# Performance work log

Measured on AMD Instinct MI355X. Metric: run time of the kernel, lower is better.

## Reference

```python
import jax, jax.numpy as jnp
import numpy as np

B, E, DM = 2, 1024, 512          # batch, n_edges, d_model
H, DK, DV = 8, 64, 64            # heads, d_k, d_v
MAX_NEIGHBOR = 5                 # == attn_max_dist
LN_EPS = 1e-6
NEG = -1e9


def setup_inputs() -> dict:
    key = jax.random.key(0)
    ks = jax.random.split(key, 9)
    s = 0.02
    return {
        "x": jax.random.normal(ks[0], (B, DM, E, 1), jnp.float32),
        "dist": jax.random.randint(ks[1], (B, E, E), 0, 12, jnp.int32),
        "base_rpr": jax.random.normal(ks[2], (MAX_NEIGHBOR + 1, DK), jnp.float32) * s,
        "w_q": jax.random.normal(ks[3], (DM, H * DK), jnp.float32) * s,
        "w_k": jax.random.normal(ks[4], (DM, H * DK), jnp.float32) * s,
        "w_v": jax.random.normal(ks[5], (DM, H * DV), jnp.float32) * s,
        "w_fc": jax.random.normal(ks[6], (H * DV, DM), jnp.float32) * s,
        "ln_g": jnp.ones((DM,), jnp.float32),
        "ln_b": jnp.zeros((DM,), jnp.float32),
    }


def reference(x, dist, base_rpr, w_q, w_k, w_v, w_fc, ln_g, ln_b):
    temp = jnp.asarray(DK, x.dtype) ** 0.5
    # local-attention mask (dist <= attn_max_dist); all edges valid (same-size meshes)
    mask = dist <= MAX_NEIGHBOR                      # [B,E,E] bool

    s = jnp.transpose(x[..., 0], (0, 2, 1))          # [B,E,DM]
    residual = s

    # LayerNorm applied to q only (as in the torch module)
    mu = s.mean(-1, keepdims=True)
    var = ((s - mu) ** 2).mean(-1, keepdims=True)
    qn = (s - mu) / jnp.sqrt(var + LN_EPS) * ln_g + ln_b

    q = (qn @ w_q).reshape(B, E, H, DK).transpose(0, 2, 1, 3)   # [B,H,E,DK]
    k = (s @ w_k).reshape(B, E, H, DK).transpose(0, 2, 1, 3)
    v = (s @ w_v).reshape(B, E, H, DV).transpose(0, 2, 1, 3)

    # relative-position representations gathered by (clipped) distance
    rpr = base_rpr[jnp.minimum(dist, MAX_NEIGHBOR)]  # [B,E,E,DK]

    qs = q / temp
    attn1 = jnp.einsum("bhid,bhjd->bhij", qs, k)
    attn2 = jnp.einsum("bhid,bijd->bhij", qs, rpr)
    logits = jnp.where(mask[:, None], attn1 + attn2, NEG)
    attn = jax.nn.softmax(logits, axis=-1)           # [B,H,E,E]

    out = jnp.einsum("bhij,bhjd->bhid", attn, v)     # [B,H,E,DV]
    out = out.transpose(0, 2, 1, 3).reshape(B, E, H * DV) @ w_fc + residual
    x_out = out.transpose(0, 2, 1)[..., None]        # [B,DM,E,1]

    mf = mask[:, None].astype(attn.dtype)            # [B,1,E,E]
    attn_per_edge = (attn * mf).sum((1, 2)) / mf.sum((1, 2))  # [B,E]
    return x_out, attn, attn_per_edge
```

## Files before the change

### kernel.cpp

```cpp
#include <hip/hip_runtime.h>

#define NB_B 2
#define NB_E 1024
#define NB_DM 512
#define NB_H 8
#define NEGV -1e9f

typedef __attribute__((ext_vector_type(8))) __bf16 bf16x8;
typedef __attribute__((ext_vector_type(8))) unsigned short u16x8;
typedef __attribute__((ext_vector_type(4))) float f32x4;

static __device__ __forceinline__ float bf2f(unsigned short u){
  union { unsigned int i; float f; } v; v.i = ((unsigned int)u) << 16; return v.f;
}
static __device__ __forceinline__ unsigned short f2bf(float f){
  union { float f; unsigned int i; } v; v.f = f;
  unsigned int r = v.i + 0x7FFFu + ((v.i >> 16) & 1u);
  return (unsigned short)(r >> 16);
}
static __device__ __forceinline__ f32x4 mfma16(bf16x8 a, bf16x8 b, f32x4 c){
  return __builtin_amdgcn_mfma_f32_16x16x32_bf16(a, b, c, 0, 0, 0);
}
static __device__ __forceinline__ float fast_exp2(float x){
#if __has_builtin(__builtin_amdgcn_exp2f)
  return __builtin_amdgcn_exp2f(x);
#else
  return exp2f(x);
#endif
}

__global__ void k_transpose_x(const float* __restrict__ x, unsigned short* __restrict__ s_bf){
  __shared__ float tile[32][33];
  const int b = blockIdx.z;
  const int d0 = blockIdx.y * 32;
  const int e0 = blockIdx.x * 32;
  const int tx = threadIdx.x, ty = threadIdx.y;
  #pragma unroll
  for (int r = 0; r < 4; ++r){
    const int d = d0 + ty + r*8;
    tile[ty + r*8][tx] = x[((size_t)b*NB_DM + d)*NB_E + e0 + tx];
  }
  __syncthreads();
  #pragma unroll
  for (int r = 0; r < 4; ++r){
    const int e = e0 + ty + r*8;
    s_bf[((size_t)b*NB_E + e)*NB_DM + d0 + tx] = f2bf(tile[tx][ty + r*8]);
  }
}

__global__ void k_transpose_w(const float* __restrict__ w0, const float* __restrict__ w1,
                              const float* __restrict__ w2, const float* __restrict__ w3,
                              unsigned short* __restrict__ wT){
  __shared__ float tile[32][33];
  const int which = blockIdx.z;
  const float* w = which==0 ? w0 : which==1 ? w1 : which==2 ? w2 : w3;
  unsigned short* dst = wT + (size_t)which*512*512;
  const int k0 = blockIdx.y*32, n0 = blockIdx.x*32;
  const int tx = threadIdx.x, ty = threadIdx.y;
  #pragma unroll
  for (int r = 0; r < 4; ++r)
    tile[ty + r*8][tx] = w[(size_t)(k0 + ty + r*8)*512 + n0 + tx];
  __syncthreads();
  #pragma unroll
  for (int r = 0; r < 4; ++r)
    dst[(size_t)(n0 + ty + r*8)*512 + k0 + tx] = f2bf(tile[tx][ty + r*8]);
}

__global__ __launch_bounds__(256) void k_ln(const unsigned short* __restrict__ s_bf,
    unsigned short* __restrict__ qn_bf, const float* __restrict__ gg, const float* __restrict__ bb){
  const int row = blockIdx.x*4 + (threadIdx.x >> 6);
  const int l = threadIdx.x & 63;
  const unsigned short* sp = s_bf + (size_t)row*512 + l*8;
  u16x8 v = *(const u16x8*)sp;
  float f[8]; float sum = 0.f, sq = 0.f;
  #pragma unroll
  for (int i = 0; i < 8; ++i){ f[i] = bf2f(v[i]); sum += f[i]; sq += f[i]*f[i]; }
  #pragma unroll
  for (int off = 32; off >= 1; off >>= 1){
    sum += __shfl_xor(sum, off);
    sq  += __shfl_xor(sq, off);
  }
  const float mu  = sum * (1.f/512.f);
  const float var = sq * (1.f/512.f) - mu*mu;
  const float rstd = rsqrtf(var + 1e-6f);
  const float4 g0 = *(const float4*)(gg + l*8);
  const float4 g1 = *(const float4*)(gg + l*8 + 4);
  const float4 b0 = *(const float4*)(bb + l*8);
  const float4 b1 = *(const float4*)(bb + l*8 + 4);
  const float gv[8] = {g0.x,g0.y,g0.z,g0.w,g1.x,g1.y,g1.z,g1.w};
  const float bv[8] = {b0.x,b0.y,b0.z,b0.w,b1.x,b1.y,b1.z,b1.w};
  u16x8 o;
  #pragma unroll
  for (int i = 0; i < 8; ++i) o[i] = f2bf((f[i]-mu)*rstd*gv[i] + bv[i]);
  *(u16x8*)(qn_bf + (size_t)row*512 + l*8) = o;
}

__global__ __launch_bounds__(256) void k_dist(const int* __restrict__ dist,
    unsigned char* __restrict__ d8, int* __restrict__ cnt){
  const int b = blockIdx.y;
  const int i0 = blockIdx.x * 16;
  const int t = threadIdx.x;
  int c0 = 0, c1 = 0, c2 = 0, c3 = 0;
  #pragma unroll 4
  for (int r = 0; r < 16; ++r){
    const int row = i0 + r;
    const int4 d = ((const int4*)(dist + ((size_t)b*NB_E + row)*NB_E))[t];
    uchar4 o;
    o.x = (unsigned char)(d.x <= 5 ? d.x : 6);
    o.y = (unsigned char)(d.y <= 5 ? d.y : 6);
    o.z = (unsigned char)(d.z <= 5 ? d.z : 6);
    o.w = (unsigned char)(d.w <= 5 ? d.w : 6);
    ((uchar4*)(d8 + ((size_t)b*NB_E + row)*NB_E))[t] = o;
    c0 += (d.x <= 5); c1 += (d.y <= 5); c2 += (d.z <= 5); c3 += (d.w <= 5);
  }
  int* cb = cnt + b*NB_E + t*4;
  atomicAdd(cb + 0, c0);
  atomicAdd(cb + 1, c1);
  atomicAdd(cb + 2, c2);
  atomicAdd(cb + 3, c3);
}

__global__ __launch_bounds__(256, 4) void k_gemm_qkv(
    const unsigned short* __restrict__ qn, const unsigned short* __restrict__ s,
    const unsigned short* __restrict__ wT, const float* __restrict__ base_rpr,
    unsigned short* __restrict__ Qb, unsigned short* __restrict__ Kb,
    unsigned short* __restrict__ VTb, float* __restrict__ qr)
{
  const int z = blockIdx.z;
  const unsigned short* A  = (z == 0) ? qn : s;
  const unsigned short* BT = wT + (size_t)z*262144;
  const int tid = threadIdx.x;
  const int l = tid & 63, wv = tid >> 6;
  const int ll = l & 15, lg = l >> 4;
  const int m0 = blockIdx.x*64 + wv*16;
  const int n0 = blockIdx.y*64;
  const unsigned short* arow = A + (size_t)(m0 + ll)*512 + lg*8;
  const unsigned short* brow = BT + (size_t)(n0 + ll)*512 + lg*8;
  f32x4 acc[4];
  #pragma unroll
  for (int nt = 0; nt < 4; ++nt) acc[nt] = (f32x4){0.f,0.f,0.f,0.f};
  bf16x8 a_c = *(const bf16x8*)(arow);
  bf16x8 b_c[4];
  #pragma unroll
  for (int nt = 0; nt < 4; ++nt) b_c[nt] = *(const bf16x8*)(brow + (size_t)nt*8192);
  #pragma unroll
  for (int ks = 0; ks < 16; ++ks){
    const int kn = (ks + 1) & 15;
    bf16x8 a_n = *(const bf16x8*)(arow + kn*32);
    bf16x8 b_n[4];
    #pragma unroll
    for (int nt = 0; nt < 4; ++nt) b_n[nt] = *(const bf16x8*)(brow + (size_t)nt*8192 + kn*32);
    #pragma unroll
    for (int nt = 0; nt < 4; ++nt) acc[nt] = mfma16(a_c, b_c[nt], acc[nt]);
    a_c = a_n;
    #pragma unroll
    for (int nt = 0; nt < 4; ++nt) b_c[nt] = b_n[nt];
  }
  const int rbase = m0 + lg*4;
  const int bidx = rbase >> 10;
  const int e = rbase & 1023;
  const int h = n0 >> 6;
  if (z == 0){
    float rprv[6][4];
    #pragma unroll
    for (int c = 0; c < 6; ++c)
      #pragma unroll
      for (int nt = 0; nt < 4; ++nt)
        rprv[c][nt] = base_rpr[c*64 + nt*16 + ll];
    #pragma unroll
    for (int nt = 0; nt < 4; ++nt){
      const int dk = nt*16 + ll;
      unsigned short* dp = Qb + (((size_t)bidx*NB_H + h)*NB_E + e)*64 + dk;
      #pragma unroll
      for (int r = 0; r < 4; ++r)
        dp[(size_t)r*64] = f2bf(acc[nt][r]*0.125f);
    }
    #pragma unroll
    for (int r = 0; r < 4; ++r){
      #pragma unroll
      for (int c = 0; c < 6; ++c){
        float tv = 0.f;
        #pragma unroll
        for (int nt = 0; nt < 4; ++nt) tv += acc[nt][r]*0.125f*rprv[c][nt];
        tv += __shfl_xor(tv, 1);
        tv += __shfl_xor(tv, 2);
        tv += __shfl_xor(tv, 4);
        tv += __shfl_xor(tv, 8);
        if (ll == 0)
          qr[(((size_t)(bidx*NB_H + h)*NB_E) + e + r)*8 + c] = tv;
      }
    }
  } else if (z == 1){
    #pragma unroll
    for (int nt = 0; nt < 4; ++nt){
      const int dk = nt*16 + ll;
      unsigned short* dp = Kb + (((size_t)bidx*NB_H + h)*NB_E + e)*64 + dk;
      #pragma unroll
      for (int r = 0; r < 4; ++r)
        dp[(size_t)r*64] = f2bf(acc[nt][r]);
    }
  } else {
    #pragma unroll
    for (int nt = 0; nt < 4; ++nt){
      const int dv = nt*16 + ll;
      ushort4 ov;
      ov.x = f2bf(acc[nt][0]); ov.y = f2bf(acc[nt][1]);
      ov.z = f2bf(acc[nt][2]); ov.w = f2bf(acc[nt][3]);
      *(ushort4*)(VTb + (((size_t)bidx*NB_H + h)*64 + dv)*NB_E + e) = ov;
    }
  }
}

__global__ __launch_bounds__(256, 4) void k_fc(
    const unsigned short* __restrict__ A, const unsigned short* __restrict__ BT,
    float* __restrict__ dst_f, const float* __restrict__ resid)
{
  const int tid = threadIdx.x;
  const int l = tid & 63, wv = tid >> 6;
  const int ll = l & 15, lg = l >> 4;
  const int m0 = blockIdx.x*64 + wv*16;
  const int n0 = blockIdx.y*32;
  const unsigned short* arow = A + (size_t)(m0 + ll)*512 + lg*8;
  const unsigned short* brow = BT + (size_t)(n0 + ll)*512 + lg*8;
  f32x4 acc[2];
  acc[0] = (f32x4){0.f,0.f,0.f,0.f};
  acc[1] = (f32x4){0.f,0.f,0.f,0.f};
  bf16x8 a_c = *(const bf16x8*)(arow);
  bf16x8 b_c0 = *(const bf16x8*)(brow);
  bf16x8 b_c1 = *(const bf16x8*)(brow + 8192);
  #pragma unroll
  for (int ks = 0; ks < 16; ++ks){
    const int kn = (ks + 1) & 15;
    bf16x8 a_n  = *(const bf16x8*)(arow + kn*32);
    bf16x8 b_n0 = *(const bf16x8*)(brow + kn*32);
    bf16x8 b_n1 = *(const bf16x8*)(brow + 8192 + kn*32);
    acc[0] = mfma16(a_c, b_c0, acc[0]);
    acc[1] = mfma16(a_c, b_c1, acc[1]);
    a_c = a_n; b_c0 = b_n0; b_c1 = b_n1;
  }
  const int rbase = m0 + lg*4;
  const int bidx = rbase >> 10;
  const int e = rbase & 1023;
  #pragma unroll
  for (int nt = 0; nt < 2; ++nt){
    const int n = n0 + nt*16 + ll;
    const float* xr = resid + ((size_t)bidx*NB_DM + n)*NB_E + e;
    const float4 rv = *(const float4*)xr;
    const float4 ov = make_float4(acc[nt][0]+rv.x, acc[nt][1]+rv.y,
                                  acc[nt][2]+rv.z, acc[nt][3]+rv.w);
    *(float4*)(dst_f + ((size_t)bidx*NB_DM + n)*NB_E + e) = ov;
  }
}

#define D_OFF 2048
#define P_OFF 18432
__global__ __launch_bounds__(256, 3) void k_attn(
    const unsigned short* __restrict__ Q, const unsigned short* __restrict__ K,
    const unsigned short* __restrict__ VT, const float* __restrict__ qr,
    const unsigned char* __restrict__ d8, float* __restrict__ attn_out,
    unsigned short* __restrict__ outb, float* __restrict__ ape_acc)
{
  __shared__ __align__(16) unsigned char smem[51200];
  unsigned short* plds = (unsigned short*)(smem + P_OFF);
  float* qr_l = (float*)smem;
  float* redm = (float*)(smem + 512);
  float* reds = (float*)(smem + 1024);

  const int tid = threadIdx.x;
  const int l = tid & 63, w = tid >> 6;
  const int lg = l >> 4, ll = l & 15;
  const int n = blockIdx.x;
  const int m = n >> 3;
  const int bh = (n & 7)*2 + (m >> 6);
  const int b = bh >> 3;
  const int ib = (m & 63) << 4;

  const unsigned char* d8g = d8 + ((size_t)b*NB_E + ib)*NB_E;
  int4 dreg[4];
  #pragma unroll
  for (int ch = 0; ch < 4; ++ch)
    dreg[ch] = ((const int4*)(d8g + (size_t)ch*4096))[tid];

  for (int t = tid; t < 16*6; t += 256)
    qr_l[t] = qr[((size_t)bh*NB_E + ib + (t/6))*8 + (t % 6)];

  const unsigned short* Qb = Q + ((size_t)bh*NB_E + ib)*64;
  bf16x8 qf[2];
  #pragma unroll
  for (int hf = 0; hf < 2; ++hf)
    qf[hf] = *(const bf16x8*)(Qb + (size_t)ll*64 + hf*32 + lg*8);

  f32x4 s[16];
  const unsigned short* Kb = K + (size_t)bh*NB_E*64;
  bf16x8 k0 = *(const bf16x8*)(Kb + (size_t)((w*16)*16 + ll)*64 + lg*8);
  bf16x8 k1 = *(const bf16x8*)(Kb + (size_t)((w*16)*16 + ll)*64 + 32 + lg*8);
  #pragma unroll
  for (int jt = 0; jt < 16; ++jt){
    const int jn = (jt + 1) & 15;
    const size_t nrow = (size_t)((w*16 + jn)*16 + ll)*64;
    bf16x8 kn0 = *(const bf16x8*)(Kb + nrow + lg*8);
    bf16x8 kn1 = *(const bf16x8*)(Kb + nrow + 32 + lg*8);
    f32x4 acc = {0.f,0.f,0.f,0.f};
    acc = mfma16(qf[0], k0, acc);
    acc = mfma16(qf[1], k1, acc);
    s[jt] = acc;
    k0 = kn0; k1 = kn1;
  }

  #pragma unroll
  for (int ch = 0; ch < 4; ++ch)
    ((int4*)(smem + D_OFF + ch*4096))[tid] = dreg[ch];
  __syncthreads();

  #pragma unroll
  for (int jt = 0; jt < 16; ++jt){
    const int j = (w*16 + jt)*16 + ll;
    #pragma unroll
    for (int r = 0; r < 4; ++r){
      const int il = lg*4 + r;
      const unsigned char c = smem[D_OFF + il*1024 + j];
      s[jt][r] = (c < 6) ? (s[jt][r] + qr_l[il*6 + c]) : NEGV;
    }
  }

  #pragma unroll
  for (int r = 0; r < 4; ++r){
    float mm = -3.0e38f;
    #pragma unroll
    for (int jt = 0; jt < 16; ++jt) mm = fmaxf(mm, s[jt][r]);
    mm = fmaxf(mm, __shfl_xor(mm, 1));
    mm = fmaxf(mm, __shfl_xor(mm, 2));
    mm = fmaxf(mm, __shfl_xor(mm, 4));
    mm = fmaxf(mm, __shfl_xor(mm, 8));
    if (ll == 0) redm[w*16 + lg*4 + r] = mm;
  }
  __syncthreads();
  float mx[4];
  #pragma unroll
  for (int r = 0; r < 4; ++r){
    const int il = lg*4 + r;
    mx[r] = fmaxf(fmaxf(redm[il], redm[16+il]), fmaxf(redm[32+il], redm[48+il]));
  }

  #pragma unroll
  for (int r = 0; r < 4; ++r){
    float sum = 0.f;
    #pragma unroll
    for (int jt = 0; jt < 16; ++jt){
      const float p = fast_exp2((s[jt][r] - mx[r]) * 1.4426950408889634f);
      s[jt][r] = p;
      sum += p;
    }
    sum += __shfl_xor(sum, 1);
    sum += __shfl_xor(sum, 2);
    sum += __shfl_xor(sum, 4);
    sum += __shfl_xor(sum, 8);
    if (ll == 0) reds[w*16 + lg*4 + r] = sum;
  }
  __syncthreads();
  float rinv[4];
  #pragma unroll
  for (int r = 0; r < 4; ++r){
    const int il = lg*4 + r;
    rinv[r] = 1.0f / (reds[il] + reds[16+il] + reds[32+il] + reds[48+il]);
  }

  #pragma unroll
  for (int jt = 0; jt < 16; ++jt){
    const int j = (w*16 + jt)*16 + ll;
    float csum = 0.f;
    #pragma unroll
    for (int r = 0; r < 4; ++r){
      const int il = lg*4 + r;
      const float pn = s[jt][r] * rinv[r];
      const int byo = ((il*1024 + j)*2) ^ ((il & 7) << 4);
      plds[byo >> 1] = f2bf(pn);
      csum += pn;
    }
    csum += __shfl_xor(csum, 16);
    csum += __shfl_xor(csum, 32);
    if (l < 16) atomicAdd(&ape_acc[(bh << 10) + j], csum);
  }
  __syncthreads();

  {
    const int il = w*4 + lg;
    float* arow = attn_out + ((size_t)bh*NB_E + ib + il)*NB_E;
    const int rowb = il*2048;
    #pragma unroll
    for (int c2 = 0; c2 < 16; ++c2){
      const int byo = (rowb + c2*128 + ll*8) ^ ((il & 7) << 4);
      const ushort4 pv = *(const ushort4*)(smem + P_OFF + byo);
      f32x4 ov;
      ov[0] = bf2f(pv.x); ov[1] = bf2f(pv.y); ov[2] = bf2f(pv.z); ov[3] = bf2f(pv.w);
      __builtin_nontemporal_store(ov, (f32x4*)(arow + c2*64 + ll*4));
    }
  }

  const unsigned short* Vb = VT + ((size_t)bh*64 + w*16 + ll)*NB_E;
  f32x4 o = {0.f,0.f,0.f,0.f};
  bf16x8 vf = *(const bf16x8*)(Vb + lg*8);
  #pragma unroll
  for (int kk = 0; kk < 32; ++kk){
    const int kn = (kk + 1) & 31;
    bf16x8 vn = *(const bf16x8*)(Vb + kn*32 + lg*8);
    const int byo = ((ll*2048 + (kk*32 + lg*8)*2)) ^ ((ll & 7) << 4);
    bf16x8 p = *(const bf16x8*)(smem + P_OFF + byo);
    o = mfma16(p, vf, o);
    vf = vn;
  }
  const int coln = (bh & 7)*64 + w*16 + ll;
  #pragma unroll
  for (int r = 0; r < 4; ++r){
    const int e0 = ib + lg*4 + r;
    outb[((size_t)b*NB_E + e0)*512 + coln] = f2bf(o[r]);
  }
}

__global__ void k_ape(const float* __restrict__ acc, const int* __restrict__ cnt,
                      float* __restrict__ out){
  const int t = blockIdx.x*256 + threadIdx.x;
  if (t < NB_B*NB_E){
    const int b = t >> 10, j = t & 1023;
    float ssum = 0.f;
    #pragma unroll
    for (int h = 0; h < 8; ++h) ssum += acc[(((b<<3) + h) << 10) + j];
    const int c = cnt[t];
    out[t] = c > 0 ? ssum / (float)c : 0.f;
  }
}

extern "C" void kernel_launch(void* const* d_in, const int* in_sizes, int n_in,
                              void* d_out, int out_size, void* d_ws, size_t ws_size,
                              hipStream_t stream)
{
  const float* x        = (const float*)d_in[0];
  const int*   dist     = (const int*)d_in[1];
  const float* base_rpr = (const float*)d_in[2];
  const float* w_q      = (const float*)d_in[3];
  const float* w_k      = (const float*)d_in[4];
  const float* w_v      = (const float*)d_in[5];
  const float* w_fc     = (const float*)d_in[6];
  const float* ln_g     = (const float*)d_in[7];
  const float* ln_b     = (const float*)d_in[8];

  float* x_out    = (float*)d_out;
  float* attn_out = x_out + (size_t)NB_B*NB_DM*NB_E;
  float* ape_out  = attn_out + (size_t)NB_B*NB_H*NB_E*NB_E;

  unsigned char* ws = (unsigned char*)d_ws;
  unsigned short* s_bf   = (unsigned short*)(ws);
  unsigned short* qn_bf  = (unsigned short*)(ws + 2097152);
  unsigned short* wT     = (unsigned short*)(ws + 4194304);
  unsigned short* Qb     = (unsigned short*)(ws + 6291456);
  unsigned short* Kb     = (unsigned short*)(ws + 8388608);
  unsigned short* VTb    = (unsigned short*)(ws + 10485760);
  unsigned short* outb   = (unsigned short*)(ws + 12582912);
  float*          qr     = (float*)(ws + 14680064);
  unsigned char*  d8     = ws + 15204352;
  int*            cnt    = (int*)(ws + 17301504);
  float*          apeacc = (float*)(ws + 17309696);

  hipMemsetAsync(cnt, 0, 8192 + 65536, stream);

  k_transpose_w<<<dim3(16,16,4), dim3(32,8), 0, stream>>>(w_q, w_k, w_v, w_fc, wT);
  k_transpose_x<<<dim3(32,16,2), dim3(32,8), 0, stream>>>(x, s_bf);
  k_ln<<<dim3(512), dim3(256), 0, stream>>>(s_bf, qn_bf, ln_g, ln_b);
  k_dist<<<dim3(64,2), dim3(256), 0, stream>>>(dist, d8, cnt);

  k_gemm_qkv<<<dim3(32,8,3), dim3(256), 0, stream>>>(qn_bf, s_bf, wT, base_rpr,
                                                     Qb, Kb, VTb, qr);

  k_attn<<<dim3(1024), dim3(256), 0, stream>>>(Qb, Kb, VTb, qr, d8, attn_out, outb, apeacc);

  k_fc<<<dim3(32,16), dim3(256), 0, stream>>>(outb, wT + 786432, x_out, x);
  k_ape<<<dim3(8), dim3(256), 0, stream>>>(apeacc, cnt, ape_out);
}
```

Before: 125.6 us.

## Replace ape atomics with per-tile partial sums and defer attn stores

Each attention block now writes its per-column probability sums to a private partial buffer instead of issuing atomicAdds to a shared accumulator. A widened k_ape then reduces the 512 partials per column. The attention-matrix write-back moves after the PV MFMA loop, which drops one barrier, and uses plain stores instead of nontemporal ones. The change removes atomic contention and a memset, but adds a 4 MB partial buffer that aliases workspace already used earlier, plus a serial reduction run by only 8 blocks.

Result: slower. 169.1 us (+34.6%).

```diff
diff --git a/kernel.cpp b/kernel.cpp
--- a/kernel.cpp
+++ b/kernel.cpp
@@ -258,7 +258,7 @@
     const unsigned short* __restrict__ Q, const unsigned short* __restrict__ K,
     const unsigned short* __restrict__ VT, const float* __restrict__ qr,
     const unsigned char* __restrict__ d8, float* __restrict__ attn_out,
-    unsigned short* __restrict__ outb, float* __restrict__ ape_acc)
+    unsigned short* __restrict__ outb, float* __restrict__ apeP)
 {
   __shared__ __align__(16) unsigned char smem[51200];
   unsigned short* plds = (unsigned short*)(smem + P_OFF);
@@ -273,7 +273,8 @@
   const int m = n >> 3;
   const int bh = (n & 7)*2 + (m >> 6);
   const int b = bh >> 3;
-  const int ib = (m & 63) << 4;
+  const int it = m & 63;
+  const int ib = it << 4;
 
   const unsigned char* d8g = d8 + ((size_t)b*NB_E + ib)*NB_E;
   int4 dreg[4];
@@ -365,6 +366,7 @@
     rinv[r] = 1.0f / (reds[il] + reds[16+il] + reds[32+il] + reds[48+il]);
   }
 
+  float* apeRow = apeP + (((size_t)bh*64 + it) << 10);
   #pragma unroll
   for (int jt = 0; jt < 16; ++jt){
     const int j = (w*16 + jt)*16 + ll;
@@ -379,23 +381,9 @@
     }
     csum += __shfl_xor(csum, 16);
     csum += __shfl_xor(csum, 32);
-    if (l < 16) atomicAdd(&ape_acc[(bh << 10) + j], csum);
-  }
-  __syncthreads();
-
-  {
-    const int il = w*4 + lg;
-    float* arow = attn_out + ((size_t)bh*NB_E + ib + il)*NB_E;
-    const int rowb = il*2048;
-    #pragma unroll
-    for (int c2 = 0; c2 < 16; ++c2){
-      const int byo = (rowb + c2*128 + ll*8) ^ ((il & 7) << 4);
-      const ushort4 pv = *(const ushort4*)(smem + P_OFF + byo);
-      f32x4 ov;
-      ov[0] = bf2f(pv.x); ov[1] = bf2f(pv.y); ov[2] = bf2f(pv.z); ov[3] = bf2f(pv.w);
-      __builtin_nontemporal_store(ov, (f32x4*)(arow + c2*64 + ll*4));
-    }
-  }
+    if (l < 16) apeRow[j] = csum;
+  }
+  __syncthreads();
 
   const unsigned short* Vb = VT + ((size_t)bh*64 + w*16 + ll)*NB_E;
   f32x4 o = {0.f,0.f,0.f,0.f};
@@ -415,19 +403,38 @@
     const int e0 = ib + lg*4 + r;
     outb[((size_t)b*NB_E + e0)*512 + coln] = f2bf(o[r]);
   }
-}
-
-__global__ void k_ape(const float* __restrict__ acc, const int* __restrict__ cnt,
-                      float* __restrict__ out){
+
+  {
+    const int il = w*4 + lg;
+    float* arow = attn_out + ((size_t)bh*NB_E + ib + il)*NB_E;
+    const int rowb = il*2048;
+    #pragma unroll
+    for (int c2 = 0; c2 < 16; ++c2){
+      const int byo = (rowb + c2*128 + ll*8) ^ ((il & 7) << 4);
+      const ushort4 pv = *(const ushort4*)(smem + P_OFF + byo);
+      f32x4 ov;
+      ov[0] = bf2f(pv.x); ov[1] = bf2f(pv.y); ov[2] = bf2f(pv.z); ov[3] = bf2f(pv.w);
+      *(f32x4*)(arow + c2*64 + ll*4) = ov;
+    }
+  }
+}
+
+__global__ __launch_bounds__(256) void k_ape(const float* __restrict__ apeP,
+    const int* __restrict__ cnt, float* __restrict__ out){
   const int t = blockIdx.x*256 + threadIdx.x;
-  if (t < NB_B*NB_E){
-    const int b = t >> 10, j = t & 1023;
-    float ssum = 0.f;
-    #pragma unroll
-    for (int h = 0; h < 8; ++h) ssum += acc[(((b<<3) + h) << 10) + j];
-    const int c = cnt[t];
-    out[t] = c > 0 ? ssum / (float)c : 0.f;
-  }
+  const int b = t >> 10, j = t & 1023;
+  float s0 = 0.f, s1 = 0.f, s2 = 0.f, s3 = 0.f;
+  const float* base = apeP + (((size_t)b*8*64) << 10) + j;
+  #pragma unroll 4
+  for (int g = 0; g < 512; g += 4){
+    s0 += base[(size_t)(g+0) << 10];
+    s1 += base[(size_t)(g+1) << 10];
+    s2 += base[(size_t)(g+2) << 10];
+    s3 += base[(size_t)(g+3) << 10];
+  }
+  const int c = cnt[t];
+  const float ssum = (s0+s1)+(s2+s3);
+  out[t] = c > 0 ? ssum / (float)c : 0.f;
 }
 
 extern "C" void kernel_launch(void* const* d_in, const int* in_sizes, int n_in,
@@ -451,6 +458,7 @@
   unsigned char* ws = (unsigned char*)d_ws;
   unsigned short* s_bf   = (unsigned short*)(ws);
   unsigned short* qn_bf  = (unsigned short*)(ws + 2097152);
+  float*          apeP   = (float*)(ws);
   unsigned short* wT     = (unsigned short*)(ws + 4194304);
   unsigned short* Qb     = (unsigned short*)(ws + 6291456);
   unsigned short* Kb     = (unsigned short*)(ws + 8388608);
@@ -459,9 +467,8 @@
   float*          qr     = (float*)(ws + 14680064);
   unsigned char*  d8     = ws + 15204352;
   int*            cnt    = (int*)(ws + 17301504);
-  float*          apeacc = (float*)(ws + 17309696);
-
-  hipMemsetAsync(cnt, 0, 8192 + 65536, stream);
+
+  hipMemsetAsync(cnt, 0, 8192, stream);
 
   k_transpose_w<<<dim3(16,16,4), dim3(32,8), 0, stream>>>(w_q, w_k, w_v, w_fc, wT);
   k_transpose_x<<<dim3(32,16,2), dim3(32,8), 0, stream>>>(x, s_bf);
@@ -471,8 +478,8 @@
   k_gemm_qkv<<<dim3(32,8,3), dim3(256), 0, stream>>>(qn_bf, s_bf, wT, base_rpr,
                                                      Qb, Kb, VTb, qr);
 
-  k_attn<<<dim3(1024), dim3(256), 0, stream>>>(Qb, Kb, VTb, qr, d8, attn_out, outb, apeacc);
+  k_attn<<<dim3(1024), dim3(256), 0, stream>>>(Qb, Kb, VTb, qr, d8, attn_out, outb, apeP);
 
   k_fc<<<dim3(32,16), dim3(256), 0, stream>>>(outb, wT + 786432, x_out, x);
-  k_ape<<<dim3(8), dim3(256), 0, stream>>>(apeacc, cnt, ape_out);
-}
+  k_ape<<<dim3(8), dim3(256), 0, stream>>>(apeP, cnt, ape_out);
+}
```

## Stage bf16 attention probabilities in workspace and expand to fp32 in separate kernel

Applied to the files above, without the earlier changes.

When the workspace is large enough, the attention kernel writes bf16 probabilities to a global scratch buffer instead of fp32 directly. A new expand kernel converts them to fp32 in the attention output and accumulates per-column sums, replacing the per-head atomics in the attention kernel. The per-batch accumulator now sums over heads directly, so k_ape simplifies. This aims to shorten the attention kernel's store-bound tail, at the cost of an extra 32MB round trip and one more launch.

Measured after the change: 212.3 us. 1.69x slower.

```diff
diff --git a/kernel.cpp b/kernel.cpp
--- a/kernel.cpp
+++ b/kernel.cpp
@@ -254,11 +254,13 @@
 
 #define D_OFF 2048
 #define P_OFF 18432
+template<bool WRITE_PG>
 __global__ __launch_bounds__(256, 3) void k_attn(
     const unsigned short* __restrict__ Q, const unsigned short* __restrict__ K,
     const unsigned short* __restrict__ VT, const float* __restrict__ qr,
     const unsigned char* __restrict__ d8, float* __restrict__ attn_out,
-    unsigned short* __restrict__ outb, float* __restrict__ ape_acc)
+    unsigned short* __restrict__ Pg, unsigned short* __restrict__ outb,
+    float* __restrict__ apeacc)
 {
   __shared__ __align__(16) unsigned char smem[51200];
   unsigned short* plds = (unsigned short*)(smem + P_OFF);
@@ -273,7 +275,8 @@
   const int m = n >> 3;
   const int bh = (n & 7)*2 + (m >> 6);
   const int b = bh >> 3;
-  const int ib = (m & 63) << 4;
+  const int it = m & 63;
+  const int ib = it << 4;
 
   const unsigned char* d8g = d8 + ((size_t)b*NB_E + ib)*NB_E;
   int4 dreg[4];
@@ -375,15 +378,28 @@
       const float pn = s[jt][r] * rinv[r];
       const int byo = ((il*1024 + j)*2) ^ ((il & 7) << 4);
       plds[byo >> 1] = f2bf(pn);
-      csum += pn;
-    }
-    csum += __shfl_xor(csum, 16);
-    csum += __shfl_xor(csum, 32);
-    if (l < 16) atomicAdd(&ape_acc[(bh << 10) + j], csum);
-  }
-  __syncthreads();
-
-  {
+      if (!WRITE_PG) csum += pn;
+    }
+    if (!WRITE_PG){
+      csum += __shfl_xor(csum, 16);
+      csum += __shfl_xor(csum, 32);
+      if (l < 16) atomicAdd(&apeacc[(b << 10) + j], csum);
+    }
+  }
+  __syncthreads();
+
+  if (WRITE_PG){
+    const int il = w*4 + lg;
+    const int gi = ib + il;
+    unsigned short* prow = Pg + (((size_t)bh << 10) + gi) * 1024;
+    const int rowb = il*2048;
+    #pragma unroll
+    for (int c2 = 0; c2 < 8; ++c2){
+      const int byo = (rowb + c2*256 + ll*16) ^ ((il & 7) << 4);
+      const u16x8 pv = *(const u16x8*)(smem + P_OFF + byo);
+      *(u16x8*)(prow + c2*128 + ll*8) = pv;
+    }
+  } else {
     const int il = w*4 + lg;
     float* arow = attn_out + ((size_t)bh*NB_E + ib + il)*NB_E;
     const int rowb = il*2048;
@@ -393,7 +409,7 @@
       const ushort4 pv = *(const ushort4*)(smem + P_OFF + byo);
       f32x4 ov;
       ov[0] = bf2f(pv.x); ov[1] = bf2f(pv.y); ov[2] = bf2f(pv.z); ov[3] = bf2f(pv.w);
-      __builtin_nontemporal_store(ov, (f32x4*)(arow + c2*64 + ll*4));
+      *(f32x4*)(arow + c2*64 + ll*4) = ov;
     }
   }
 
@@ -417,16 +433,51 @@
   }
 }
 
-__global__ void k_ape(const float* __restrict__ acc, const int* __restrict__ cnt,
+__global__ __launch_bounds__(256) void k_expand(const unsigned short* __restrict__ Pg,
+    float* __restrict__ attn, float* __restrict__ apeacc)
+{
+  __shared__ float psum[256][9];
+  const int bh = blockIdx.y, tile = blockIdx.x, tid = threadIdx.x;
+  const int b = bh >> 3;
+  const size_t rowbase = ((size_t)bh << 10) + tile*32;
+  const unsigned short* src = Pg + (rowbase << 10);
+  float* dst = attn + (rowbase << 10);
+  const int tcol = (tid & 127) * 8;
+  const int trow = tid >> 7;
+  float acc[8];
+  #pragma unroll
+  for (int k = 0; k < 8; ++k) acc[k] = 0.f;
+  #pragma unroll 4
+  for (int loop = 0; loop < 16; ++loop){
+    const int row = loop*2 + trow;
+    const u16x8 v = *(const u16x8*)(src + ((size_t)row << 10) + tcol);
+    f32x4 o0, o1;
+    #pragma unroll
+    for (int k = 0; k < 4; ++k){
+      const float f0 = bf2f(v[k]);
+      const float f1 = bf2f(v[4+k]);
+      o0[k] = f0; o1[k] = f1;
+      acc[k] += f0; acc[4+k] += f1;
+    }
+    *(f32x4*)(dst + ((size_t)row << 10) + tcol) = o0;
+    *(f32x4*)(dst + ((size_t)row << 10) + tcol + 4) = o1;
+  }
+  #pragma unroll
+  for (int k = 0; k < 8; ++k) psum[tid][k] = acc[k];
+  __syncthreads();
+  if (tid < 128){
+    #pragma unroll
+    for (int k = 0; k < 8; ++k)
+      atomicAdd(&apeacc[(b << 10) + tid*8 + k], psum[tid][k] + psum[tid+128][k]);
+  }
+}
+
+__global__ void k_ape(const float* __restrict__ apeacc, const int* __restrict__ cnt,
                       float* __restrict__ out){
   const int t = blockIdx.x*256 + threadIdx.x;
   if (t < NB_B*NB_E){
-    const int b = t >> 10, j = t & 1023;
-    float ssum = 0.f;
-    #pragma unroll
-    for (int h = 0; h < 8; ++h) ssum += acc[(((b<<3) + h) << 10) + j];
     const int c = cnt[t];
-    out[t] = c > 0 ? ssum / (float)c : 0.f;
+    out[t] = c > 0 ? apeacc[t] / (float)c : 0.f;
   }
 }
 
@@ -460,8 +511,11 @@
   unsigned char*  d8     = ws + 15204352;
   int*            cnt    = (int*)(ws + 17301504);
   float*          apeacc = (float*)(ws + 17309696);
-
-  hipMemsetAsync(cnt, 0, 8192 + 65536, stream);
+  const size_t    PG_OFF = 17825792;
+  unsigned short* Pg     = (unsigned short*)(ws + PG_OFF);
+  const bool big_ws = ws_size >= PG_OFF + (size_t)33554432;
+
+  hipMemsetAsync(cnt, 0, 16384, stream);
 
   k_transpose_w<<<dim3(16,16,4), dim3(32,8), 0, stream>>>(w_q, w_k, w_v, w_fc, wT);
   k_transpose_x<<<dim3(32,16,2), dim3(32,8), 0, stream>>>(x, s_bf);
@@ -471,7 +525,14 @@
   k_gemm_qkv<<<dim3(32,8,3), dim3(256), 0, stream>>>(qn_bf, s_bf, wT, base_rpr,
                                                      Qb, Kb, VTb, qr);
 
-  k_attn<<<dim3(1024), dim3(256), 0, stream>>>(Qb, Kb, VTb, qr, d8, attn_out, outb, apeacc);
+  if (big_ws){
+    k_attn<true><<<dim3(1024), dim3(256), 0, stream>>>(Qb, Kb, VTb, qr, d8,
+                                                       attn_out, Pg, outb, apeacc);
+    k_expand<<<dim3(32,16), dim3(256), 0, stream>>>(Pg, attn_out, apeacc);
+  } else {
+    k_attn<false><<<dim3(1024), dim3(256), 0, stream>>>(Qb, Kb, VTb, qr, d8,
+                                                        attn_out, Pg, outb, apeacc);
+  }
 
   k_fc<<<dim3(32,16), dim3(256), 0, stream>>>(outb, wT + 786432, x_out, x);
   k_ape<<<dim3(8), dim3(256), 0, stream>>>(apeacc, cnt, ape_out);
```

## Restructure attention kernel to 8-row tiles with 512 threads and no max pass

Applied to the files above, without the earlier changes.

The attention kernel now processes 8 query rows per block with 512 threads (8 waves each covering 128 key columns) instead of 16 rows with 256 threads, doubling the grid and halving shared memory. The row-max reduction pass is removed: exponentials are taken directly on masked logits, which relies on logits being small, and a tiny epsilon guards the sum. Half of each MFMA tile is wasted on duplicated rows, and only four waves do the PV product. Attention writes switch from nontemporal to plain stores, and global loads lose their software prefetch.

Result: slower. 149.5 us (+19.0%).

```diff
diff --git a/kernel.cpp b/kernel.cpp
--- a/kernel.cpp
+++ b/kernel.cpp
@@ -4,7 +4,6 @@
 #define NB_E 1024
 #define NB_DM 512
 #define NB_H 8
-#define NEGV -1e9f
 
 typedef __attribute__((ext_vector_type(8))) __bf16 bf16x8;
 typedef __attribute__((ext_vector_type(8))) unsigned short u16x8;
@@ -252,168 +251,140 @@
   }
 }
 
-#define D_OFF 2048
-#define P_OFF 18432
-__global__ __launch_bounds__(256, 3) void k_attn(
+#define D_OFF 1024
+#define P_OFF 10240
+__global__ __launch_bounds__(512, 8) void k_attn(
     const unsigned short* __restrict__ Q, const unsigned short* __restrict__ K,
     const unsigned short* __restrict__ VT, const float* __restrict__ qr,
     const unsigned char* __restrict__ d8, float* __restrict__ attn_out,
-    unsigned short* __restrict__ outb, float* __restrict__ ape_acc)
+    unsigned short* __restrict__ outb, float* __restrict__ apeacc16)
 {
-  __shared__ __align__(16) unsigned char smem[51200];
+  __shared__ __align__(16) unsigned char smem[26624];
   unsigned short* plds = (unsigned short*)(smem + P_OFF);
   float* qr_l = (float*)smem;
-  float* redm = (float*)(smem + 512);
-  float* reds = (float*)(smem + 1024);
+  float* reds = (float*)(smem + 256);
 
   const int tid = threadIdx.x;
   const int l = tid & 63, w = tid >> 6;
   const int lg = l >> 4, ll = l & 15;
   const int n = blockIdx.x;
   const int m = n >> 3;
-  const int bh = (n & 7)*2 + (m >> 6);
+  const int bh = (n & 7)*2 + (m >> 7);
   const int b = bh >> 3;
-  const int ib = (m & 63) << 4;
+  const int ib = (m & 127) << 3;
+  const int j0 = w << 7;
 
   const unsigned char* d8g = d8 + ((size_t)b*NB_E + ib)*NB_E;
-  int4 dreg[4];
-  #pragma unroll
-  for (int ch = 0; ch < 4; ++ch)
-    dreg[ch] = ((const int4*)(d8g + (size_t)ch*4096))[tid];
-
-  for (int t = tid; t < 16*6; t += 256)
-    qr_l[t] = qr[((size_t)bh*NB_E + ib + (t/6))*8 + (t % 6)];
-
-  const unsigned short* Qb = Q + ((size_t)bh*NB_E + ib)*64;
-  bf16x8 qf[2];
-  #pragma unroll
-  for (int hf = 0; hf < 2; ++hf)
-    qf[hf] = *(const bf16x8*)(Qb + (size_t)ll*64 + hf*32 + lg*8);
-
-  f32x4 s[16];
+  const int4 dr0 = ((const int4*)d8g)[tid];
+  ((int4*)(smem + D_OFF))[tid] = dr0;
+
+  if (tid < 48)
+    qr_l[tid] = qr[((size_t)bh*NB_E + ib + (tid/6))*8 + (tid % 6)];
+
+  const unsigned short* Qbp = Q + ((size_t)bh*NB_E + ib)*64;
+  bf16x8 qf0 = *(const bf16x8*)(Qbp + (size_t)(ll & 7)*64 + lg*8);
+  bf16x8 qf1 = *(const bf16x8*)(Qbp + (size_t)(ll & 7)*64 + 32 + lg*8);
+
+  f32x4 s[8];
   const unsigned short* Kb = K + (size_t)bh*NB_E*64;
-  bf16x8 k0 = *(const bf16x8*)(Kb + (size_t)((w*16)*16 + ll)*64 + lg*8);
-  bf16x8 k1 = *(const bf16x8*)(Kb + (size_t)((w*16)*16 + ll)*64 + 32 + lg*8);
-  #pragma unroll
-  for (int jt = 0; jt < 16; ++jt){
-    const int jn = (jt + 1) & 15;
-    const size_t nrow = (size_t)((w*16 + jn)*16 + ll)*64;
-    bf16x8 kn0 = *(const bf16x8*)(Kb + nrow + lg*8);
-    bf16x8 kn1 = *(const bf16x8*)(Kb + nrow + 32 + lg*8);
+  #pragma unroll
+  for (int jt = 0; jt < 8; ++jt){
+    const size_t krow = (size_t)(j0 + jt*16 + ll)*64;
+    bf16x8 k0 = *(const bf16x8*)(Kb + krow + lg*8);
+    bf16x8 k1 = *(const bf16x8*)(Kb + krow + 32 + lg*8);
     f32x4 acc = {0.f,0.f,0.f,0.f};
-    acc = mfma16(qf[0], k0, acc);
-    acc = mfma16(qf[1], k1, acc);
+    acc = mfma16(qf0, k0, acc);
+    acc = mfma16(qf1, k1, acc);
     s[jt] = acc;
-    k0 = kn0; k1 = kn1;
-  }
-
-  #pragma unroll
-  for (int ch = 0; ch < 4; ++ch)
-    ((int4*)(smem + D_OFF + ch*4096))[tid] = dreg[ch];
+  }
   __syncthreads();
 
-  #pragma unroll
-  for (int jt = 0; jt < 16; ++jt){
-    const int j = (w*16 + jt)*16 + ll;
+  if (lg < 2){
+    float rsum[4] = {0.f, 0.f, 0.f, 0.f};
+    #pragma unroll
+    for (int jt = 0; jt < 8; ++jt){
+      const int j = j0 + jt*16 + ll;
+      #pragma unroll
+      for (int r = 0; r < 4; ++r){
+        const int il = lg*4 + r;
+        const unsigned char c = smem[D_OFF + il*1024 + j];
+        const float p = (c < 6)
+          ? fast_exp2((s[jt][r] + qr_l[il*6 + c]) * 1.4426950408889634f) : 0.f;
+        s[jt][r] = p;
+        rsum[r] += p;
+      }
+    }
+    #pragma unroll
+    for (int r = 0; r < 4; ++r){
+      float sum = rsum[r];
+      sum += __shfl_xor(sum, 1);
+      sum += __shfl_xor(sum, 2);
+      sum += __shfl_xor(sum, 4);
+      sum += __shfl_xor(sum, 8);
+      if (ll == 0) reds[w*8 + lg*4 + r] = sum;
+    }
+  }
+  __syncthreads();
+
+  if (lg < 2){
+    float rinv[4];
     #pragma unroll
     for (int r = 0; r < 4; ++r){
       const int il = lg*4 + r;
-      const unsigned char c = smem[D_OFF + il*1024 + j];
-      s[jt][r] = (c < 6) ? (s[jt][r] + qr_l[il*6 + c]) : NEGV;
-    }
-  }
-
-  #pragma unroll
-  for (int r = 0; r < 4; ++r){
-    float mm = -3.0e38f;
-    #pragma unroll
-    for (int jt = 0; jt < 16; ++jt) mm = fmaxf(mm, s[jt][r]);
-    mm = fmaxf(mm, __shfl_xor(mm, 1));
-    mm = fmaxf(mm, __shfl_xor(mm, 2));
-    mm = fmaxf(mm, __shfl_xor(mm, 4));
-    mm = fmaxf(mm, __shfl_xor(mm, 8));
-    if (ll == 0) redm[w*16 + lg*4 + r] = mm;
+      float tot = 0.f;
+      #pragma unroll
+      for (int wv = 0; wv < 8; ++wv) tot += reds[wv*8 + il];
+      rinv[r] = 1.0f / (tot + 1e-30f);
+    }
+    #pragma unroll
+    for (int jt = 0; jt < 8; ++jt){
+      const int j = j0 + jt*16 + ll;
+      float csum = 0.f;
+      #pragma unroll
+      for (int r = 0; r < 4; ++r){
+        const int il = lg*4 + r;
+        const float pn = s[jt][r] * rinv[r];
+        const int byo = ((il*1024 + j)*2) ^ (il << 4);
+        plds[byo >> 1] = f2bf(pn);
+        csum += pn;
+      }
+      csum += __shfl_xor(csum, 16);
+      if (lg == 0) atomicAdd(&apeacc16[(bh << 10) + j], csum);
+    }
   }
   __syncthreads();
-  float mx[4];
-  #pragma unroll
-  for (int r = 0; r < 4; ++r){
-    const int il = lg*4 + r;
-    mx[r] = fmaxf(fmaxf(redm[il], redm[16+il]), fmaxf(redm[32+il], redm[48+il]));
-  }
-
-  #pragma unroll
-  for (int r = 0; r < 4; ++r){
-    float sum = 0.f;
-    #pragma unroll
-    for (int jt = 0; jt < 16; ++jt){
-      const float p = fast_exp2((s[jt][r] - mx[r]) * 1.4426950408889634f);
-      s[jt][r] = p;
-      sum += p;
-    }
-    sum += __shfl_xor(sum, 1);
-    sum += __shfl_xor(sum, 2);
-    sum += __shfl_xor(sum, 4);
-    sum += __shfl_xor(sum, 8);
-    if (ll == 0) reds[w*16 + lg*4 + r] = sum;
-  }
-  __syncthreads();
-  float rinv[4];
-  #pragma unroll
-  for (int r = 0; r < 4; ++r){
-    const int il = lg*4 + r;
-    rinv[r] = 1.0f / (reds[il] + reds[16+il] + reds[32+il] + reds[48+il]);
-  }
-
-  #pragma unroll
-  for (int jt = 0; jt < 16; ++jt){
-    const int j = (w*16 + jt)*16 + ll;
-    float csum = 0.f;
-    #pragma unroll
-    for (int r = 0; r < 4; ++r){
-      const int il = lg*4 + r;
-      const float pn = s[jt][r] * rinv[r];
-      const int byo = ((il*1024 + j)*2) ^ ((il & 7) << 4);
-      plds[byo >> 1] = f2bf(pn);
-      csum += pn;
-    }
-    csum += __shfl_xor(csum, 16);
-    csum += __shfl_xor(csum, 32);
-    if (l < 16) atomicAdd(&ape_acc[(bh << 10) + j], csum);
-  }
-  __syncthreads();
+
+  if (w < 4){
+    const unsigned short* Vb = VT + ((size_t)bh*64 + w*16 + ll)*NB_E;
+    f32x4 o = {0.f,0.f,0.f,0.f};
+    #pragma unroll 4
+    for (int kk = 0; kk < 32; ++kk){
+      bf16x8 vf = *(const bf16x8*)(Vb + kk*32 + lg*8);
+      const int byo = (((ll & 7)*1024 + kk*32 + lg*8)*2) ^ ((ll & 7) << 4);
+      bf16x8 p = *(const bf16x8*)(smem + P_OFF + byo);
+      o = mfma16(p, vf, o);
+    }
+    if (lg < 2){
+      const int coln = (bh & 7)*64 + w*16 + ll;
+      #pragma unroll
+      for (int r = 0; r < 4; ++r){
+        const int e0 = ib + lg*4 + r;
+        outb[((size_t)b*NB_E + e0)*512 + coln] = f2bf(o[r]);
+      }
+    }
+  }
 
   {
-    const int il = w*4 + lg;
-    float* arow = attn_out + ((size_t)bh*NB_E + ib + il)*NB_E;
-    const int rowb = il*2048;
-    #pragma unroll
-    for (int c2 = 0; c2 < 16; ++c2){
-      const int byo = (rowb + c2*128 + ll*8) ^ ((il & 7) << 4);
+    float* arow = attn_out + ((size_t)bh*NB_E + ib + w)*NB_E;
+    #pragma unroll
+    for (int c2 = 0; c2 < 4; ++c2){
+      const int col = c2*256 + l*4;
+      const int byo = ((w*1024 + col)*2) ^ (w << 4);
       const ushort4 pv = *(const ushort4*)(smem + P_OFF + byo);
       f32x4 ov;
       ov[0] = bf2f(pv.x); ov[1] = bf2f(pv.y); ov[2] = bf2f(pv.z); ov[3] = bf2f(pv.w);
-      __builtin_nontemporal_store(ov, (f32x4*)(arow + c2*64 + ll*4));
-    }
-  }
-
-  const unsigned short* Vb = VT + ((size_t)bh*64 + w*16 + ll)*NB_E;
-  f32x4 o = {0.f,0.f,0.f,0.f};
-  bf16x8 vf = *(const bf16x8*)(Vb + lg*8);
-  #pragma unroll
-  for (int kk = 0; kk < 32; ++kk){
-    const int kn = (kk + 1) & 31;
-    bf16x8 vn = *(const bf16x8*)(Vb + kn*32 + lg*8);
-    const int byo = ((ll*2048 + (kk*32 + lg*8)*2)) ^ ((ll & 7) << 4);
-    bf16x8 p = *(const bf16x8*)(smem + P_OFF + byo);
-    o = mfma16(p, vf, o);
-    vf = vn;
-  }
-  const int coln = (bh & 7)*64 + w*16 + ll;
-  #pragma unroll
-  for (int r = 0; r < 4; ++r){
-    const int e0 = ib + lg*4 + r;
-    outb[((size_t)b*NB_E + e0)*512 + coln] = f2bf(o[r]);
+      *(f32x4*)(arow + col) = ov;
+    }
   }
 }
 
@@ -459,9 +430,9 @@
   float*          qr     = (float*)(ws + 14680064);
   unsigned char*  d8     = ws + 15204352;
   int*            cnt    = (int*)(ws + 17301504);
-  float*          apeacc = (float*)(ws + 17309696);
-
-  hipMemsetAsync(cnt, 0, 8192 + 65536, stream);
+  float*          ape16  = (float*)(ws + 17309696);
+
+  (void)hipMemsetAsync(cnt, 0, 8192 + 65536, stream);
 
   k_transpose_w<<<dim3(16,16,4), dim3(32,8), 0, stream>>>(w_q, w_k, w_v, w_fc, wT);
   k_transpose_x<<<dim3(32,16,2), dim3(32,8), 0, stream>>>(x, s_bf);
@@ -471,8 +442,9 @@
   k_gemm_qkv<<<dim3(32,8,3), dim3(256), 0, stream>>>(qn_bf, s_bf, wT, base_rpr,
                                                      Qb, Kb, VTb, qr);
 
-  k_attn<<<dim3(1024), dim3(256), 0, stream>>>(Qb, Kb, VTb, qr, d8, attn_out, outb, apeacc);
+  k_attn<<<dim3(2048), dim3(512), 0, stream>>>(Qb, Kb, VTb, qr, d8,
+                                               attn_out, outb, ape16);
 
   k_fc<<<dim3(32,16), dim3(256), 0, stream>>>(outb, wT + 786432, x_out, x);
-  k_ape<<<dim3(8), dim3(256), 0, stream>>>(apeacc, cnt, ape_out);
-}
+  k_ape<<<dim3(8), dim3(256), 0, stream>>>(ape16, cnt, ape_out);
+}
```
